# Kernel tuning notes

Measured on AMD Instinct MI355X. Metric: run time of the kernel, lower is better.

The kernel has to match this reference:

```python
import jax, jax.numpy as jnp
import numpy as np

B, D, H, W = 16, 64, 64, 64
K = 1024


def setup_inputs() -> dict:
    key = jax.random.key(0)
    k1, k2 = jax.random.split(key)
    x = jax.random.normal(k1, (B, D, H, W), dtype=jnp.float32)
    limit = 3.0 ** 0.5
    e_i_ts = jax.random.uniform(k2, (D, K), dtype=jnp.float32, minval=-limit, maxval=limit)
    return {"x": x, "e_i_ts": e_i_ts}


def reference(x, e_i_ts):
    b, d, h, w = x.shape
    # [B,H,W,D] -> [N,D]
    flat_x = jnp.transpose(x, (0, 2, 3, 1)).reshape(-1, d)
    distances = (
        jnp.sum(flat_x * flat_x, axis=1, keepdims=True)
        - 2.0 * (flat_x @ e_i_ts)
        + jnp.sum(e_i_ts * e_i_ts, axis=0, keepdims=True)
    )
    encoding_indices = jnp.argmin(distances, axis=1)  # [N]
    reshaped_indices = encoding_indices.reshape(b, h, w)
    # codebook gather: e_i_ts.T is [K,D]
    quantized = jnp.take(e_i_ts.T, reshaped_indices, axis=0)  # [B,H,W,D]
    quantized_x = jnp.transpose(quantized, (0, 3, 1, 2))  # [B,D,H,W]

    dictionary_loss = jnp.mean((jax.lax.stop_gradient(x) - quantized_x) ** 2)
    commitment_loss = jnp.mean((x - jax.lax.stop_gradient(quantized_x)) ** 2)
    # straight-through estimator
    quantized_x = x + jax.lax.stop_gradient(quantized_x - x)
    return quantized_x, dictionary_loss, commitment_loss, encoding_indices.reshape(b, -1)
```

## Files before the change

### kernel.cpp

```cpp
#include <hip/hip_runtime.h>

#define DD 64
#define KK 1024
#define NPTS 65536
#define TOTAL 4194304

#define OFF_L1 4194304
#define OFF_L2 4194305
#define OFF_IDX 4194306

#define WS_ENH_F 64
#define WS_EHT_BYTE 65536
#define WS_ELT_BYTE (65536 + 131072)

#define MARGIN_S 0.006f

typedef __attribute__((ext_vector_type(8))) short short8;
typedef __attribute__((ext_vector_type(4))) float f32x4;

__device__ __forceinline__ unsigned short bf16_rne(float f) {
    unsigned b = __float_as_uint(f);
    return (unsigned short)((b + 0x7FFFu + ((b >> 16) & 1u)) >> 16);
}
__device__ __forceinline__ float bf16_to_f(unsigned short h) {
    return __uint_as_float(((unsigned)h) << 16);
}
__device__ __forceinline__ unsigned umax(unsigned a, unsigned b) { return a > b ? a : b; }
__device__ __forceinline__ unsigned umin(unsigned a, unsigned b) { return a < b ? a : b; }
__device__ __forceinline__ void gld_lds16(const void* g, void* l) {
    __builtin_amdgcn_global_load_lds(
        (const __attribute__((address_space(1))) void*)g,
        (__attribute__((address_space(3))) void*)l, 16, 0, 0);
}
__device__ __forceinline__ int swz(int r, int d) {
    return ((d & ~7) ^ ((r & 7) << 3)) | (d & 7);
}

__global__ __launch_bounds__(256) void prep_kernel(const float* __restrict__ e,
                                                   float* __restrict__ enh,
                                                   unsigned short* __restrict__ ehT,
                                                   unsigned short* __restrict__ elT,
                                                   float* __restrict__ sum,
                                                   unsigned* __restrict__ tick) {
    const int tid = threadIdx.x;
    if (blockIdx.x == 0 && tid == 0) { *sum = 0.f; *tick = 0u; }
    const int wave = tid >> 6, lane = tid & 63;
    const int k = blockIdx.x * 4 + wave;
    const float v = e[lane * KK + k];
    const unsigned short h = bf16_rne(v);
    const unsigned short l = bf16_rne(v - bf16_to_f(h));
    const int pos = k * 64 + swz(k, lane);
    ehT[pos] = h;
    elT[pos] = l;
    float s2 = v * v;
#pragma unroll
    for (int m = 32; m > 0; m >>= 1) s2 += __shfl_down(s2, m, 64);
    if (lane == 0) enh[k] = 512.0f - 0.5f * s2;
}

__global__ __launch_bounds__(256) void vq_gemm(const float* __restrict__ x,
                                               const float* __restrict__ e,
                                               const float* __restrict__ enh,
                                               const unsigned short* __restrict__ ehT,
                                               const unsigned short* __restrict__ elT,
                                               float* __restrict__ out,
                                               float* __restrict__ sum,
                                               unsigned* __restrict__ tick) {
    __shared__ __align__(16) char ebuf[2 * 16384];
    __shared__ float xnp4[256];

    float* mv1 = (float*)ebuf;
    float* mv2 = mv1 + 128;
    int*   mi1 = (int*)(mv2 + 128);
    int*   ks  = mi1 + 128;
    float* lv  = (float*)(ks + 64);
    float* xp  = lv + 64;
    int*   rl  = (int*)(xp + 64);
    int*   rn  = rl + 64;
    float* rv  = (float*)(rn + 1);
    int*   ri  = (int*)(rv + 4);

    const int tid = threadIdx.x;
    const int wave = tid >> 6, lane = tid & 63;
    const int n0 = blockIdx.x * 64;
    const int b = n0 >> 12;
    const int hw0 = n0 & 4095;

    const char* ehTb = (const char*)ehT;
    const char* elTb = (const char*)elT;
    const int lofs = wave * 1024 + lane * 16;

    {
        char* db = ebuf;
        gld_lds16(ehTb + lofs,        db + wave * 1024);
        gld_lds16(ehTb + 4096 + lofs, db + 4096 + wave * 1024);
        gld_lds16(elTb + lofs,        db + 8192 + wave * 1024);
        gld_lds16(elTb + 4096 + lofs, db + 12288 + wave * 1024);
    }

    unsigned short* xbh = (unsigned short*)(ebuf + 16384);
    unsigned short* xbl = xbh + 4096;
    {
        const float* xs = x + ((b * DD + wave * 16) << 12) + hw0 + lane;
        float xv[16];
        float xn = 0.f;
#pragma unroll
        for (int s = 0; s < 16; ++s) {
            xv[s] = xs[s << 12];
            xn = fmaf(xv[s], xv[s], xn);
        }
        xnp4[tid] = xn;
#pragma unroll
        for (int g = 0; g < 2; ++g) {
            short8 hh, ll;
#pragma unroll
            for (int j = 0; j < 8; ++j) {
                const float f = xv[g * 8 + j];
                const unsigned short h = bf16_rne(f);
                hh[j] = (short)h;
                ll[j] = (short)bf16_rne(f - bf16_to_f(h));
            }
            const int pos = lane * 64 + ((wave * 16 + g * 8) ^ ((lane & 7) << 3));
            *(short8*)(xbh + pos) = hh;
            *(short8*)(xbl + pos) = ll;
        }
    }
    __syncthreads();

    const int ln15 = lane & 15, q8 = (lane >> 4) * 8;
    const int wp = (wave >> 1) * 32;
    const int wc = (wave & 1) * 32;

    short8 ah[2][2], al[2][2];
#pragma unroll
    for (int rf = 0; rf < 2; ++rf)
#pragma unroll
        for (int kc = 0; kc < 2; ++kc) {
            const int pp = wp + rf * 16 + ln15;
            const int pos = pp * 64 + ((kc * 32 + q8) ^ ((pp & 7) << 3));
            ah[rf][kc] = *(const short8*)(xbh + pos);
            al[rf][kc] = *(const short8*)(xbl + pos);
        }

    unsigned v1u[8], v2u[8];
#pragma unroll
    for (int r = 0; r < 8; ++r) { v1u[r] = 0u; v2u[r] = 0u; }

    for (int kt = 0; kt < 16; ++kt) {
        __syncthreads();
        if (kt < 15) {
            const int nkt = kt + 1;
            char* db = ebuf + (nkt & 1) * 16384;
            const char* sH = ehTb + nkt * 8192 + lofs;
            const char* sL = elTb + nkt * 8192 + lofs;
            gld_lds16(sH,        db + wave * 1024);
            gld_lds16(sH + 4096, db + 4096 + wave * 1024);
            gld_lds16(sL,        db + 8192 + wave * 1024);
            gld_lds16(sL + 4096, db + 12288 + wave * 1024);
        }
        const unsigned short* ebH = (const unsigned short*)(ebuf + (kt & 1) * 16384);
        const unsigned short* ebL = ebH + 4096;

        f32x4 acc[2][2];
#pragma unroll
        for (int cf = 0; cf < 2; ++cf) {
            const float ec = enh[kt * 64 + wc + cf * 16 + ln15];
#pragma unroll
            for (int rf = 0; rf < 2; ++rf)
                acc[rf][cf] = (f32x4){ec, ec, ec, ec};
        }

#pragma unroll
        for (int kc = 0; kc < 2; ++kc) {
            short8 bh[2], bl[2];
#pragma unroll
            for (int cf = 0; cf < 2; ++cf) {
                const int c = wc + cf * 16 + ln15;
                const int pos = c * 64 + ((kc * 32 + q8) ^ ((c & 7) << 3));
                bh[cf] = *(const short8*)(ebH + pos);
                bl[cf] = *(const short8*)(ebL + pos);
            }
#pragma unroll
            for (int rf = 0; rf < 2; ++rf)
#pragma unroll
                for (int cf = 0; cf < 2; ++cf) {
                    acc[rf][cf] = __builtin_amdgcn_mfma_f32_16x16x32_bf16(al[rf][kc], bh[cf], acc[rf][cf], 0, 0, 0);
                    acc[rf][cf] = __builtin_amdgcn_mfma_f32_16x16x32_bf16(ah[rf][kc], bl[cf], acc[rf][cf], 0, 0, 0);
                    acc[rf][cf] = __builtin_amdgcn_mfma_f32_16x16x32_bf16(ah[rf][kc], bh[cf], acc[rf][cf], 0, 0, 0);
                }
        }

#pragma unroll
        for (int rf = 0; rf < 2; ++rf)
#pragma unroll
            for (int reg = 0; reg < 4; ++reg) {
                const int r = rf * 4 + reg;
                const unsigned k0 = (__float_as_uint(acc[rf][0][reg]) | 31u) ^ (unsigned)(kt * 2 + 0);
                const unsigned k1 = (__float_as_uint(acc[rf][1][reg]) | 31u) ^ (unsigned)(kt * 2 + 1);
                const unsigned a = umax(k0, k1), bb = umin(k0, k1);
                v2u[r] = umax(umax(v2u[r], umin(v1u[r], a)), bb);
                v1u[r] = umax(v1u[r], a);
            }
    }

    __syncthreads();
    if (tid == 0) *rn = 0;

#pragma unroll
    for (int r = 0; r < 8; ++r) {
        const unsigned c5 = 31u - (v1u[r] & 31u);
        int col = (int)(c5 >> 1) * 64 + wc + (int)(c5 & 1) * 16 + ln15;
        float val = __uint_as_float(v1u[r] & ~31u);
        float sec = __uint_as_float(v2u[r] & ~31u);
#pragma unroll
        for (int msk = 1; msk < 16; msk <<= 1) {
            const float ov = __shfl_xor(val, msk);
            const int oc = __shfl_xor(col, msk);
            const float os = __shfl_xor(sec, msk);
            sec = fmaxf(fmaxf(sec, os), fminf(val, ov));
            const bool t = (ov > val) || (ov == val && oc < col);
            val = t ? ov : val;
            col = t ? oc : col;
        }
        if (ln15 == 0) {
            const int q = lane >> 4;
            const int h = wave & 1;
            const int pt = wp + (r >> 2) * 16 + q * 4 + (r & 3);
            mv1[pt * 2 + h] = val;
            mi1[pt * 2 + h] = col;
            mv2[pt * 2 + h] = sec;
        }
    }
    __syncthreads();
    if (tid < 64) {
        const float va = mv1[tid * 2], vb = mv1[tid * 2 + 1];
        const int ia = mi1[tid * 2], ib = mi1[tid * 2 + 1];
        const bool t = (vb > va) || (vb == va && ib < ia);
        const float bv = t ? vb : va;
        const int bi = t ? ib : ia;
        const float sec = fmaxf(fmaxf(mv2[tid * 2], mv2[tid * 2 + 1]), fminf(va, vb));
        ks[tid] = bi;
        const float xnp = xnp4[tid] + xnp4[64 + tid] + xnp4[128 + tid] + xnp4[192 + tid];
        const float bmid = __uint_as_float(__float_as_uint(bv) | 16u);
        lv[tid] = xnp + 1024.0f - 2.0f * bmid;
        if (bv - sec < MARGIN_S) {
            const int w = atomicAdd(rn, 1);
            rl[w] = tid;
        }
    }
    __syncthreads();

    const int lcnt = *rn;
    for (int it = 0; it < lcnt; ++it) {
        const int pr = rl[it];
        if (tid < 64) xp[tid] = x[((b * DD + tid) << 12) + hw0 + pr];
        __syncthreads();
        float d0 = 0.f, d1 = 0.f, d2 = 0.f, d3 = 0.f;
#pragma unroll 8
        for (int dd = 0; dd < DD; ++dd) {
            const float xd = xp[dd];
            const float4 ev = *(const float4*)(e + dd * KK + tid * 4);
            d0 = fmaf(xd, ev.x, d0);
            d1 = fmaf(xd, ev.y, d1);
            d2 = fmaf(xd, ev.z, d2);
            d3 = fmaf(xd, ev.w, d3);
        }
        const float4 ea = *(const float4*)(enh + tid * 4);
        float bs = d0 + ea.x;
        int bi2 = tid * 4;
        if (d1 + ea.y > bs) { bs = d1 + ea.y; bi2 = tid * 4 + 1; }
        if (d2 + ea.z > bs) { bs = d2 + ea.z; bi2 = tid * 4 + 2; }
        if (d3 + ea.w > bs) { bs = d3 + ea.w; bi2 = tid * 4 + 3; }
#pragma unroll
        for (int m = 1; m < 64; m <<= 1) {
            const float ov = __shfl_xor(bs, m, 64);
            const int oi = __shfl_xor(bi2, m, 64);
            if (ov > bs || (ov == bs && oi < bi2)) { bs = ov; bi2 = oi; }
        }
        if (lane == 0) { rv[wave] = bs; ri[wave] = bi2; }
        __syncthreads();
        if (tid == 0) {
            float gs = rv[0];
            int gi = ri[0];
#pragma unroll
            for (int t2 = 1; t2 < 4; ++t2)
                if (rv[t2] > gs || (rv[t2] == gs && ri[t2] < gi)) { gs = rv[t2]; gi = ri[t2]; }
            ks[pr] = gi;
            const float xnp = xnp4[pr] + xnp4[64 + pr] + xnp4[128 + pr] + xnp4[192 + pr];
            lv[pr] = xnp + 1024.0f - 2.0f * gs;
        }
        __syncthreads();
    }

    if (tid < 64) {
        out[OFF_IDX + n0 + tid] = (float)ks[tid];
        float lc = lv[tid];
#pragma unroll
        for (int off = 32; off > 0; off >>= 1) lc += __shfl_down(lc, off, 64);
        if (tid == 0) {
            atomicAdd(sum, lc);
            __threadfence();
            const unsigned old = atomicAdd(tick, 1u);
            if (old == (unsigned)(gridDim.x - 1)) {
                const float s = atomicAdd(sum, 0.0f);
                const float m = s * (1.0f / (float)TOTAL);
                out[OFF_L1] = m;
                out[OFF_L2] = m;
            }
        }
    }

    {
        const int pe = tid & 63, dqr = tid >> 6;
        const int kp = ks[pe];
        const int kx = (kp & 7) << 3;
        float qa[16];
#pragma unroll
        for (int g = 0; g < 2; ++g) {
            const int pos = kp * 64 + ((dqr * 16 + g * 8) ^ kx);
            const short8 h8 = *(const short8*)(ehT + pos);
            const short8 l8 = *(const short8*)(elT + pos);
#pragma unroll
            for (int j = 0; j < 8; ++j)
                qa[g * 8 + j] = bf16_to_f((unsigned short)h8[j]) + bf16_to_f((unsigned short)l8[j]);
        }
        float* ob = out + ((b * DD + dqr * 16) << 12) + hw0 + pe;
#pragma unroll
        for (int s = 0; s < 16; ++s) ob[s << 12] = qa[s];
    }
}

extern "C" void kernel_launch(void* const* d_in, const int* in_sizes, int n_in,
                              void* d_out, int out_size, void* d_ws, size_t ws_size,
                              hipStream_t stream) {
    const float* x = (const float*)d_in[0];
    const float* e = (const float*)d_in[1];
    float* out = (float*)d_out;

    float* sum = (float*)d_ws;
    unsigned* tick = (unsigned*)d_ws + 2;
    float* enh = (float*)d_ws + WS_ENH_F;
    unsigned short* ehT = (unsigned short*)((char*)d_ws + WS_EHT_BYTE);
    unsigned short* elT = (unsigned short*)((char*)d_ws + WS_ELT_BYTE);

    prep_kernel<<<256, 256, 0, stream>>>(e, enh, ehT, elT, sum, tick);
    vq_gemm<<<NPTS / 64, 256, 0, stream>>>(x, e, enh, ehT, elT, out, sum, tick);
}
```

Baseline: 137.9 us.

## Double points per block so each wave covers all 64 codebook columns

Each block now handles 128 points instead of 64, and each wave takes 32 points across all 64 codes of a tile. Before, the four waves split points and codes in a 2x2 grid. Each codebook tile loaded into LDS is therefore reused across twice as many points, and the cross-wave merge of argmin candidates is removed. The packed index field grows to 6 bits and the near-tie margin is widened slightly. In exchange the kernel needs more registers and LDS per block and launches half as many blocks, and the extra low bits taken from the float key may send more points to the exact fallback path.

```diff
diff --git a/kernel.cpp b/kernel.cpp
--- a/kernel.cpp
+++ b/kernel.cpp
@@ -13,7 +13,7 @@
 #define WS_EHT_BYTE 65536
 #define WS_ELT_BYTE (65536 + 131072)
 
-#define MARGIN_S 0.006f
+#define MARGIN_S 0.008f
 
 typedef __attribute__((ext_vector_type(8))) short short8;
 typedef __attribute__((ext_vector_type(4))) float f32x4;
@@ -67,22 +67,23 @@
                                                float* __restrict__ sum,
                                                unsigned* __restrict__ tick) {
     __shared__ __align__(16) char ebuf[2 * 16384];
-    __shared__ float xnp4[256];
-
-    float* mv1 = (float*)ebuf;
-    float* mv2 = mv1 + 128;
-    int*   mi1 = (int*)(mv2 + 128);
-    int*   ks  = mi1 + 128;
-    float* lv  = (float*)(ks + 64);
-    float* xp  = lv + 64;
+    __shared__ __align__(16) char xbuf[32768];
+    __shared__ float xnp2[256];
+
+    unsigned short* xbh = (unsigned short*)xbuf;
+    unsigned short* xbl = xbh + 128 * 64;
+    int*   ks  = (int*)xbuf;
+    float* lv  = (float*)(ks + 128);
+    float* xp  = lv + 128;
     int*   rl  = (int*)(xp + 64);
-    int*   rn  = rl + 64;
+    int*   rn  = rl + 128;
     float* rv  = (float*)(rn + 1);
     int*   ri  = (int*)(rv + 4);
+    float* red = (float*)(ri + 4);
 
     const int tid = threadIdx.x;
     const int wave = tid >> 6, lane = tid & 63;
-    const int n0 = blockIdx.x * 64;
+    const int n0 = blockIdx.x * 128;
     const int b = n0 >> 12;
     const int hw0 = n0 & 4095;
 
@@ -98,20 +99,19 @@
         gld_lds16(elTb + 4096 + lofs, db + 12288 + wave * 1024);
     }
 
-    unsigned short* xbh = (unsigned short*)(ebuf + 16384);
-    unsigned short* xbl = xbh + 4096;
     {
-        const float* xs = x + ((b * DD + wave * 16) << 12) + hw0 + lane;
-        float xv[16];
+        const int p = tid & 127, dg = tid >> 7;
+        const float* xs = x + ((b * DD + dg * 32) << 12) + hw0 + p;
+        float xv[32];
         float xn = 0.f;
 #pragma unroll
-        for (int s = 0; s < 16; ++s) {
+        for (int s = 0; s < 32; ++s) {
             xv[s] = xs[s << 12];
             xn = fmaf(xv[s], xv[s], xn);
         }
-        xnp4[tid] = xn;
-#pragma unroll
-        for (int g = 0; g < 2; ++g) {
+        xnp2[tid] = xn;
+#pragma unroll
+        for (int g = 0; g < 4; ++g) {
             short8 hh, ll;
 #pragma unroll
             for (int j = 0; j < 8; ++j) {
@@ -120,7 +120,8 @@
                 hh[j] = (short)h;
                 ll[j] = (short)bf16_rne(f - bf16_to_f(h));
             }
-            const int pos = lane * 64 + ((wave * 16 + g * 8) ^ ((lane & 7) << 3));
+            const int d0 = dg * 32 + g * 8;
+            const int pos = p * 64 + (d0 ^ ((p & 7) << 3));
             *(short8*)(xbh + pos) = hh;
             *(short8*)(xbl + pos) = ll;
         }
@@ -128,8 +129,7 @@
     __syncthreads();
 
     const int ln15 = lane & 15, q8 = (lane >> 4) * 8;
-    const int wp = (wave >> 1) * 32;
-    const int wc = (wave & 1) * 32;
+    const int wp = wave * 32;
 
     short8 ah[2][2], al[2][2];
 #pragma unroll
@@ -161,10 +161,10 @@
         const unsigned short* ebH = (const unsigned short*)(ebuf + (kt & 1) * 16384);
         const unsigned short* ebL = ebH + 4096;
 
-        f32x4 acc[2][2];
-#pragma unroll
-        for (int cf = 0; cf < 2; ++cf) {
-            const float ec = enh[kt * 64 + wc + cf * 16 + ln15];
+        f32x4 acc[2][4];
+#pragma unroll
+        for (int cf = 0; cf < 4; ++cf) {
+            const float ec = enh[kt * 64 + cf * 16 + ln15];
 #pragma unroll
             for (int rf = 0; rf < 2; ++rf)
                 acc[rf][cf] = (f32x4){ec, ec, ec, ec};
@@ -172,10 +172,10 @@
 
 #pragma unroll
         for (int kc = 0; kc < 2; ++kc) {
-            short8 bh[2], bl[2];
-#pragma unroll
-            for (int cf = 0; cf < 2; ++cf) {
-                const int c = wc + cf * 16 + ln15;
+            short8 bh[4], bl[4];
+#pragma unroll
+            for (int cf = 0; cf < 4; ++cf) {
+                const int c = cf * 16 + ln15;
                 const int pos = c * 64 + ((kc * 32 + q8) ^ ((c & 7) << 3));
                 bh[cf] = *(const short8*)(ebH + pos);
                 bl[cf] = *(const short8*)(ebL + pos);
@@ -183,7 +183,7 @@
 #pragma unroll
             for (int rf = 0; rf < 2; ++rf)
 #pragma unroll
-                for (int cf = 0; cf < 2; ++cf) {
+                for (int cf = 0; cf < 4; ++cf) {
                     acc[rf][cf] = __builtin_amdgcn_mfma_f32_16x16x32_bf16(al[rf][kc], bh[cf], acc[rf][cf], 0, 0, 0);
                     acc[rf][cf] = __builtin_amdgcn_mfma_f32_16x16x32_bf16(ah[rf][kc], bl[cf], acc[rf][cf], 0, 0, 0);
                     acc[rf][cf] = __builtin_amdgcn_mfma_f32_16x16x32_bf16(ah[rf][kc], bh[cf], acc[rf][cf], 0, 0, 0);
@@ -195,9 +195,14 @@
 #pragma unroll
             for (int reg = 0; reg < 4; ++reg) {
                 const int r = rf * 4 + reg;
-                const unsigned k0 = (__float_as_uint(acc[rf][0][reg]) | 31u) ^ (unsigned)(kt * 2 + 0);
-                const unsigned k1 = (__float_as_uint(acc[rf][1][reg]) | 31u) ^ (unsigned)(kt * 2 + 1);
-                const unsigned a = umax(k0, k1), bb = umin(k0, k1);
+                const unsigned k0 = (__float_as_uint(acc[rf][0][reg]) | 63u) ^ (unsigned)(kt * 4 + 0);
+                const unsigned k1 = (__float_as_uint(acc[rf][1][reg]) | 63u) ^ (unsigned)(kt * 4 + 1);
+                const unsigned k2 = (__float_as_uint(acc[rf][2][reg]) | 63u) ^ (unsigned)(kt * 4 + 2);
+                const unsigned k3 = (__float_as_uint(acc[rf][3][reg]) | 63u) ^ (unsigned)(kt * 4 + 3);
+                unsigned a = umax(k0, k1), bb = umin(k0, k1);
+                v2u[r] = umax(umax(v2u[r], umin(v1u[r], a)), bb);
+                v1u[r] = umax(v1u[r], a);
+                a = umax(k2, k3); bb = umin(k2, k3);
                 v2u[r] = umax(umax(v2u[r], umin(v1u[r], a)), bb);
                 v1u[r] = umax(v1u[r], a);
             }
@@ -205,13 +210,14 @@
 
     __syncthreads();
     if (tid == 0) *rn = 0;
+    __syncthreads();
 
 #pragma unroll
     for (int r = 0; r < 8; ++r) {
-        const unsigned c5 = 31u - (v1u[r] & 31u);
-        int col = (int)(c5 >> 1) * 64 + wc + (int)(c5 & 1) * 16 + ln15;
-        float val = __uint_as_float(v1u[r] & ~31u);
-        float sec = __uint_as_float(v2u[r] & ~31u);
+        const unsigned c6 = 63u - (v1u[r] & 63u);
+        int col = (int)(c6 >> 2) * 64 + (int)(c6 & 3) * 16 + ln15;
+        float val = __uint_as_float(v1u[r] & ~63u);
+        float sec = __uint_as_float(v2u[r] & ~63u);
 #pragma unroll
         for (int msk = 1; msk < 16; msk <<= 1) {
             const float ov = __shfl_xor(val, msk);
@@ -224,28 +230,15 @@
         }
         if (ln15 == 0) {
             const int q = lane >> 4;
-            const int h = wave & 1;
             const int pt = wp + (r >> 2) * 16 + q * 4 + (r & 3);
-            mv1[pt * 2 + h] = val;
-            mi1[pt * 2 + h] = col;
-            mv2[pt * 2 + h] = sec;
-        }
-    }
-    __syncthreads();
-    if (tid < 64) {
-        const float va = mv1[tid * 2], vb = mv1[tid * 2 + 1];
-        const int ia = mi1[tid * 2], ib = mi1[tid * 2 + 1];
-        const bool t = (vb > va) || (vb == va && ib < ia);
-        const float bv = t ? vb : va;
-        const int bi = t ? ib : ia;
-        const float sec = fmaxf(fmaxf(mv2[tid * 2], mv2[tid * 2 + 1]), fminf(va, vb));
-        ks[tid] = bi;
-        const float xnp = xnp4[tid] + xnp4[64 + tid] + xnp4[128 + tid] + xnp4[192 + tid];
-        const float bmid = __uint_as_float(__float_as_uint(bv) | 16u);
-        lv[tid] = xnp + 1024.0f - 2.0f * bmid;
-        if (bv - sec < MARGIN_S) {
-            const int w = atomicAdd(rn, 1);
-            rl[w] = tid;
+            ks[pt] = col;
+            const float xnp = xnp2[pt] + xnp2[128 + pt];
+            const float bmid = __uint_as_float(__float_as_uint(val) | 32u);
+            lv[pt] = xnp + 1024.0f - 2.0f * bmid;
+            if (val - sec < MARGIN_S) {
+                const int w = atomicAdd(rn, 1);
+                rl[w] = pt;
+            }
         }
     }
     __syncthreads();
@@ -286,47 +279,49 @@
             for (int t2 = 1; t2 < 4; ++t2)
                 if (rv[t2] > gs || (rv[t2] == gs && ri[t2] < gi)) { gs = rv[t2]; gi = ri[t2]; }
             ks[pr] = gi;
-            const float xnp = xnp4[pr] + xnp4[64 + pr] + xnp4[128 + pr] + xnp4[192 + pr];
+            const float xnp = xnp2[pr] + xnp2[128 + pr];
             lv[pr] = xnp + 1024.0f - 2.0f * gs;
         }
         __syncthreads();
     }
 
-    if (tid < 64) {
+    if (tid < 128) {
         out[OFF_IDX + n0 + tid] = (float)ks[tid];
         float lc = lv[tid];
 #pragma unroll
         for (int off = 32; off > 0; off >>= 1) lc += __shfl_down(lc, off, 64);
-        if (tid == 0) {
-            atomicAdd(sum, lc);
-            __threadfence();
-            const unsigned old = atomicAdd(tick, 1u);
-            if (old == (unsigned)(gridDim.x - 1)) {
-                const float s = atomicAdd(sum, 0.0f);
-                const float m = s * (1.0f / (float)TOTAL);
-                out[OFF_L1] = m;
-                out[OFF_L2] = m;
-            }
+        if (lane == 0) red[wave] = lc;
+    }
+    __syncthreads();
+    if (tid == 0) {
+        atomicAdd(sum, red[0] + red[1]);
+        __threadfence();
+        const unsigned old = atomicAdd(tick, 1u);
+        if (old == (unsigned)(gridDim.x - 1)) {
+            const float s = atomicAdd(sum, 0.0f);
+            const float m = s * (1.0f / (float)TOTAL);
+            out[OFF_L1] = m;
+            out[OFF_L2] = m;
         }
     }
 
     {
-        const int pe = tid & 63, dqr = tid >> 6;
+        const int pe = tid & 127, dh = tid >> 7;
         const int kp = ks[pe];
         const int kx = (kp & 7) << 3;
-        float qa[16];
-#pragma unroll
-        for (int g = 0; g < 2; ++g) {
-            const int pos = kp * 64 + ((dqr * 16 + g * 8) ^ kx);
+        float qa[32];
+#pragma unroll
+        for (int g = 0; g < 4; ++g) {
+            const int pos = kp * 64 + ((dh * 32 + g * 8) ^ kx);
             const short8 h8 = *(const short8*)(ehT + pos);
             const short8 l8 = *(const short8*)(elT + pos);
 #pragma unroll
             for (int j = 0; j < 8; ++j)
                 qa[g * 8 + j] = bf16_to_f((unsigned short)h8[j]) + bf16_to_f((unsigned short)l8[j]);
         }
-        float* ob = out + ((b * DD + dqr * 16) << 12) + hw0 + pe;
-#pragma unroll
-        for (int s = 0; s < 16; ++s) ob[s << 12] = qa[s];
+        float* ob = out + ((b * DD + dh * 32) << 12) + hw0 + pe;
+#pragma unroll
+        for (int s = 0; s < 32; ++s) ob[s << 12] = qa[s];
     }
 }
 
@@ -344,5 +339,5 @@
     unsigned short* elT = (unsigned short*)((char*)d_ws + WS_ELT_BYTE);
 
     prep_kernel<<<256, 256, 0, stream>>>(e, enh, ehT, elT, sum, tick);
-    vq_gemm<<<NPTS / 64, 256, 0, stream>>>(x, e, enh, ehT, elT, out, sum, tick);
-}
+    vq_gemm<<<NPTS / 128, 256, 0, stream>>>(x, e, enh, ehT, elT, out, sum, tick);
+}
```

New measurement: 124.6 us. 1.11x faster.
